# Kernel tuning notes

Hardware: AMD Instinct MI355X
Metric: run time of the kernel (lower is better)

Reference implementation:

```python
import jax, jax.numpy as jnp
import numpy as np
from jax import lax

B = 1024
D_VQ = 64
KS = 1024
KX = 1024
BETA = 0.25


def _conv1d(x, w, b):
    # x: [N, Cin, L], w: [Cout, Cin, 3], 'same' padding
    y = lax.conv_general_dilated(x, w, (1,), [(1, 1)], dimension_numbers=('NCH', 'OIH', 'NCH'))
    return y + b[None, :, None]


def _conv2d(x, w, b):
    # x: [N, Cin, H, W], w: [Cout, Cin, 3, 3], 'same' padding
    y = lax.conv_general_dilated(x, w, (1, 1), [(1, 1), (1, 1)], dimension_numbers=('NCHW', 'OIHW', 'NCHW'))
    return y + b[None, :, None, None]


def _gelu(x):
    return jax.nn.gelu(x, approximate=False)


def _vq_ema(z_e, codebook, beta):
    # z_e: [N, D], codebook: [K, D]
    d = (jnp.sum(z_e * z_e, axis=1, keepdims=True)
         - 2.0 * (z_e @ codebook.T)
         + jnp.sum(codebook * codebook, axis=1)[None, :])  # [N, K]
    idx = jnp.argmin(d, axis=1)                              # [N]
    z_q = codebook[idx]                                      # gather [N, D]
    vq_loss = beta * jnp.mean((z_e - lax.stop_gradient(z_q)) ** 2)
    z_q_st = z_e + lax.stop_gradient(z_q - z_e)              # straight-through
    n = z_e.shape[0]
    probs = jnp.zeros((codebook.shape[0],), z_e.dtype).at[idx].add(1.0) / n
    perplexity = jnp.exp(-jnp.sum(probs * jnp.log(probs + 1e-10)))
    return z_q_st, idx, vq_loss, perplexity


def setup_inputs() -> dict:
    key = jax.random.key(0)
    ks = iter(jax.random.split(key, 40))

    def p(shape, s=0.05):
        return jax.random.normal(next(ks), shape, jnp.float32) * s

    inp = {
        'cubes': jax.random.normal(next(ks), (B, 9, 8, 72), jnp.float32),
        # spectral encoder
        's_w1': p((16, 1, 3)), 's_b1': jnp.zeros((16,), jnp.float32),
        's_w2': p((16, 16, 3)), 's_b2': jnp.zeros((16,), jnp.float32),
        's_fc_w': p((D_VQ, 16 * 8)), 's_fc_b': jnp.zeros((D_VQ,), jnp.float32),
        'cb_s': p((KS, D_VQ), 1.0),
        # spectral decoder
        's_dec_fc_w': p((16 * 8, D_VQ)), 's_dec_fc_b': jnp.zeros((16 * 8,), jnp.float32),
        's_dec_w1': p((16, 16, 3)), 's_dec_b1': jnp.zeros((16,), jnp.float32),
        's_dec_w2': p((1, 16, 3)), 's_dec_b2': jnp.zeros((1,), jnp.float32),
        # spatial encoder
        'x_w1': p((16, 8, 3, 3)), 'x_b1': jnp.zeros((16,), jnp.float32),
        'x_w2': p((16, 16, 3, 3)), 'x_b2': jnp.zeros((16,), jnp.float32),
        'x_fc_w': p((D_VQ, 16 * 3 * 3)), 'x_fc_b': jnp.zeros((D_VQ,), jnp.float32),
        'cb_x': p((KX, D_VQ), 1.0),
        # spatial decoder
        'x_dec_fc_w': p((16 * 3 * 3, D_VQ)), 'x_dec_fc_b': jnp.zeros((16 * 3 * 3,), jnp.float32),
        'x_dec_w1': p((16, 16, 3, 3)), 'x_dec_b1': jnp.zeros((16,), jnp.float32),
        'x_dec_w2': p((8, 16, 3, 3)), 'x_dec_b2': jnp.zeros((8,), jnp.float32),
        'return_recon': 1,
    }
    return inp


def reference(cubes, s_w1, s_b1, s_w2, s_b2, s_fc_w, s_fc_b, cb_s,
              s_dec_fc_w, s_dec_fc_b, s_dec_w1, s_dec_b1, s_dec_w2, s_dec_b2,
              x_w1, x_b1, x_w2, x_b2, x_fc_w, x_fc_b, cb_x,
              x_dec_fc_w, x_dec_fc_b, x_dec_w1, x_dec_b1, x_dec_w2, x_dec_b2,
              return_recon):
    b, p, t, f = cubes.shape
    n = b * p * t
    c6 = cubes.reshape(b, p, t, 8, 3, 3)                   # [B,P,T,8,3,3]
    cperm = jnp.transpose(c6, (0, 1, 2, 4, 5, 3))          # [B,P,T,3,3,8]

    # --- spectral path ---
    spec = jnp.mean(cperm, axis=(3, 4))                    # [B,P,T,8]
    spec_seq = spec.reshape(n, 1, 8)
    s = _gelu(_conv1d(spec_seq, s_w1, s_b1))
    s = _gelu(_conv1d(s, s_w2, s_b2))
    z_e_s = s.reshape(n, 16 * 8) @ s_fc_w.T + s_fc_b       # [N,D]
    z_q_s, k_idx, vq_loss_s, perplex_s = _vq_ema(z_e_s, cb_s, BETA)
    emb_s = z_q_s.reshape(b, p, t, D_VQ)
    k_idx = k_idx.reshape(b, p, t)

    # --- spatial path ---
    spatial = c6.reshape(n, 8, 3, 3)
    x = _gelu(_conv2d(spatial, x_w1, x_b1))
    x = _gelu(_conv2d(x, x_w2, x_b2))
    z_e_x = x.reshape(n, 16 * 9) @ x_fc_w.T + x_fc_b
    z_q_x, m_idx, vq_loss_x, perplex_x = _vq_ema(z_e_x, cb_x, BETA)
    emb_x = z_q_x.reshape(b, p, t, D_VQ)
    m_idx = m_idx.reshape(b, p, t)

    total = vq_loss_s + vq_loss_x

    if return_recon:
        s_dec = (z_q_s @ s_dec_fc_w.T + s_dec_fc_b).reshape(n, 16, 8)
        s_dec = _gelu(_conv1d(s_dec, s_dec_w1, s_dec_b1))
        recon_s = _conv1d(s_dec, s_dec_w2, s_dec_b2)[:, 0, :].reshape(b, p, t, 8)
        recon_loss_s = jnp.mean((recon_s - spec) ** 2)

        x_dec = (z_q_x @ x_dec_fc_w.T + x_dec_fc_b).reshape(n, 16, 3, 3)
        x_dec = _gelu(_conv2d(x_dec, x_dec_w1, x_dec_b1))
        recon_x = _conv2d(x_dec, x_dec_w2, x_dec_b2)        # [N,8,3,3]
        recon_loss_x = jnp.mean((recon_x - spatial) ** 2)
        recon_loss_total = recon_loss_s + recon_loss_x
    else:
        recon_loss_total = jnp.float32(0.0)

    return (emb_s, emb_x, k_idx, m_idx, total, perplex_s, perplex_x, recon_loss_total)
```

## Files before the change

### kernel.cpp

```cpp
#include <hip/hip_runtime.h>
#include <math.h>

#define NTOK 73728

__device__ __forceinline__ float gelu_f(float x) {
    return 0.5f * x * (1.0f + erff(x * 0.70710678118654752440f));
}

__global__ void k_norms(const float* __restrict__ cb_s, const float* __restrict__ cb_x,
                        double* __restrict__ cn_s, double* __restrict__ cn_x) {
    int i = blockIdx.x * blockDim.x + threadIdx.x;
    if (i >= 2048) return;
    const float* cb = (i < 1024) ? cb_s : cb_x;
    double* cn = (i < 1024) ? cn_s : cn_x;
    int c = i & 1023;
    double s = 0.0;
    for (int k = 0; k < 64; ++k) { double v = (double)cb[c * 64 + k]; s += v * v; }
    cn[c] = s;
}

__global__ void k_transpose(const float* __restrict__ src, float* __restrict__ dst, int E) {
    int i = blockIdx.x * 256 + threadIdx.x;
    if (i >= 64 * E) return;
    int e = i >> 6, d = i & 63;
    dst[i] = src[d * E + e];
}

__global__ void k_weff_s(const float* __restrict__ w1, const float* __restrict__ b1,
                         const float* __restrict__ dfcw, const float* __restrict__ dfcb,
                         float* __restrict__ weffT, float* __restrict__ beff) {
    int idx = blockIdx.x * 256 + threadIdx.x;
    if (idx >= 128 * 64) return;
    int o = idx >> 6, d = idx & 63;
    int c = o >> 3, l = o & 7;
    double acc = 0.0;
    for (int ci = 0; ci < 16; ++ci)
        for (int dd = 0; dd < 3; ++dd) {
            int ll = l + dd - 1;
            if (ll < 0 || ll > 7) continue;
            acc += (double)w1[(c * 16 + ci) * 3 + dd] * (double)dfcw[(ci * 8 + ll) * 64 + d];
        }
    weffT[d * 132 + o] = (float)acc;
    if (o < 4) weffT[d * 132 + 128 + o] = 0.f;
    if (d == 0) {
        double bb = (double)b1[c];
        for (int ci = 0; ci < 16; ++ci)
            for (int dd = 0; dd < 3; ++dd) {
                int ll = l + dd - 1;
                if (ll < 0 || ll > 7) continue;
                bb += (double)w1[(c * 16 + ci) * 3 + dd] * (double)dfcb[ci * 8 + ll];
            }
        beff[o] = (float)bb;
    }
}

__global__ void k_weff_x(const float* __restrict__ w1, const float* __restrict__ b1,
                         const float* __restrict__ dfcw, const float* __restrict__ dfcb,
                         float* __restrict__ weffT, float* __restrict__ beff) {
    int idx = blockIdx.x * 256 + threadIdx.x;
    if (idx >= 144 * 64) return;
    int o = idx >> 6, d = idx & 63;
    int c = o / 9, p = o - c * 9;
    int i = p / 3, j = p % 3;
    double acc = 0.0;
    for (int ci = 0; ci < 16; ++ci)
        for (int di = 0; di < 3; ++di) {
            int ii = i + di - 1; if (ii < 0 || ii > 2) continue;
            for (int dj = 0; dj < 3; ++dj) {
                int jj = j + dj - 1; if (jj < 0 || jj > 2) continue;
                acc += (double)w1[((c * 16 + ci) * 3 + di) * 3 + dj]
                     * (double)dfcw[(ci * 9 + ii * 3 + jj) * 64 + d];
            }
        }
    weffT[d * 148 + o] = (float)acc;
    if (o < 4) weffT[d * 148 + 144 + o] = 0.f;
    if (d == 0) {
        double bb = (double)b1[c];
        for (int ci = 0; ci < 16; ++ci)
            for (int di = 0; di < 3; ++di) {
                int ii = i + di - 1; if (ii < 0 || ii > 2) continue;
                for (int dj = 0; dj < 3; ++dj) {
                    int jj = j + dj - 1; if (jj < 0 || jj > 2) continue;
                    bb += (double)w1[((c * 16 + ci) * 3 + di) * 3 + dj]
                        * (double)dfcb[ci * 9 + ii * 3 + jj];
                }
            }
        beff[o] = (float)bb;
    }
}

__global__ void __launch_bounds__(256) k_spec_enc(
    const float* __restrict__ cubes,
    const float* __restrict__ w1, const float* __restrict__ b1,
    const float* __restrict__ w2, const float* __restrict__ b2,
    const float* __restrict__ fcwT, const float* __restrict__ fcb,
    float* __restrict__ z_out)
{
    __shared__ float S[16 * 8];
    __shared__ float A[16 * 136];
    __shared__ float Bb[16 * 136];
    int tid = threadIdx.x;
    int t = tid >> 4, c = tid & 15;
    if (tid < 128) {
        int tk = tid >> 3, f = tid & 7;
        const float* cu = cubes + ((size_t)blockIdx.x * 16 + tk) * 72 + f * 9;
        float s = 0.f;
        #pragma unroll
        for (int k = 0; k < 9; ++k) s += cu[k];
        S[tk * 8 + f] = s * (1.0f / 9.0f);
    }
    __syncthreads();
    {
        float s0[8];
        *(float4*)&s0[0] = *(const float4*)&S[t * 8];
        *(float4*)&s0[4] = *(const float4*)&S[t * 8 + 4];
        float wa = w1[c * 3 + 0], wb = w1[c * 3 + 1], wc = w1[c * 3 + 2], bb = b1[c];
        #pragma unroll
        for (int l = 0; l < 8; ++l) {
            float v = fmaf(wb, s0[l], bb);
            if (l > 0) v = fmaf(wa, s0[l - 1], v);
            if (l < 7) v = fmaf(wc, s0[l + 1], v);
            A[t * 136 + c * 8 + l] = gelu_f(v);
        }
    }
    __syncthreads();
    {
        float acc[8];
        #pragma unroll
        for (int l = 0; l < 8; ++l) acc[l] = b2[c];
        for (int ci = 0; ci < 16; ++ci) {
            float r[8];
            *(float4*)&r[0] = *(const float4*)&A[t * 136 + ci * 8];
            *(float4*)&r[4] = *(const float4*)&A[t * 136 + ci * 8 + 4];
            float wa = w2[(c * 16 + ci) * 3 + 0], wb = w2[(c * 16 + ci) * 3 + 1], wc = w2[(c * 16 + ci) * 3 + 2];
            #pragma unroll
            for (int l = 0; l < 8; ++l) {
                if (l > 0) acc[l] = fmaf(wa, r[l - 1], acc[l]);
                acc[l] = fmaf(wb, r[l], acc[l]);
                if (l < 7) acc[l] = fmaf(wc, r[l + 1], acc[l]);
            }
        }
        #pragma unroll
        for (int l = 0; l < 8; ++l) Bb[t * 136 + c * 8 + l] = gelu_f(acc[l]);
    }
    __syncthreads();
    {
        float4 zv = make_float4(fcb[c * 4 + 0], fcb[c * 4 + 1], fcb[c * 4 + 2], fcb[c * 4 + 3]);
        #pragma unroll 4
        for (int e = 0; e < 128; ++e) {
            float be = Bb[t * 136 + e];
            float4 wv = *(const float4*)(fcwT + (e << 6) + (c << 2));
            zv.x = fmaf(wv.x, be, zv.x);
            zv.y = fmaf(wv.y, be, zv.y);
            zv.z = fmaf(wv.z, be, zv.z);
            zv.w = fmaf(wv.w, be, zv.w);
        }
        *(float4*)(z_out + ((size_t)blockIdx.x * 16 + t) * 64 + c * 4) = zv;
    }
}

__global__ void __launch_bounds__(256) k_spat_enc(
    const float* __restrict__ cubes,
    const float* __restrict__ w1, const float* __restrict__ b1,
    const float* __restrict__ w2, const float* __restrict__ b2,
    const float* __restrict__ fcwT, const float* __restrict__ fcb,
    float* __restrict__ z_out)
{
    __shared__ float A[16 * 200];
    __shared__ float Bb[16 * 200];
    int tid = threadIdx.x;
    int t = tid >> 4, c = tid & 15;
    for (int u = tid; u < 1152; u += 256) {
        int tk = u / 72, e = u - tk * 72;
        int ci = e / 9, p = e - ci * 9;
        A[tk * 200 + ci * 12 + p] = cubes[(size_t)blockIdx.x * 1152 + u];
    }
    __syncthreads();
    {
        float acc[9];
        #pragma unroll
        for (int p = 0; p < 9; ++p) acc[p] = b1[c];
        for (int ci = 0; ci < 8; ++ci) {
            float r[12];
            *(float4*)&r[0] = *(const float4*)&A[t * 200 + ci * 12];
            *(float4*)&r[4] = *(const float4*)&A[t * 200 + ci * 12 + 4];
            *(float4*)&r[8] = *(const float4*)&A[t * 200 + ci * 12 + 8];
            const float* w = w1 + (c * 8 + ci) * 9;
            #pragma unroll
            for (int p = 0; p < 9; ++p) {
                int i = p / 3, j = p % 3;
                #pragma unroll
                for (int di = 0; di < 3; ++di) {
                    int ii = i + di - 1; if (ii < 0 || ii > 2) continue;
                    #pragma unroll
                    for (int dj = 0; dj < 3; ++dj) {
                        int jj = j + dj - 1; if (jj < 0 || jj > 2) continue;
                        acc[p] = fmaf(w[di * 3 + dj], r[ii * 3 + jj], acc[p]);
                    }
                }
            }
        }
        #pragma unroll
        for (int p = 0; p < 9; ++p) Bb[t * 200 + c * 12 + p] = gelu_f(acc[p]);
    }
// ... 9 lines not shown
            *(float4*)&r[8] = *(const float4*)&Bb[t * 200 + ci * 12 + 8];
            const float* w = w2 + (c * 16 + ci) * 9;
            #pragma unroll
            for (int p = 0; p < 9; ++p) {
                int i = p / 3, j = p % 3;
                #pragma unroll
                for (int di = 0; di < 3; ++di) {
                    int ii = i + di - 1; if (ii < 0 || ii > 2) continue;
                    #pragma unroll
                    for (int dj = 0; dj < 3; ++dj) {
                        int jj = j + dj - 1; if (jj < 0 || jj > 2) continue;
                        acc[p] = fmaf(w[di * 3 + dj], r[ii * 3 + jj], acc[p]);
                    }
                }
            }
        }
        __syncthreads();
        #pragma unroll
        for (int p = 0; p < 9; ++p) A[t * 200 + c * 12 + p] = gelu_f(acc[p]);
    }
    __syncthreads();
    {
        float4 zv = make_float4(fcb[c * 4 + 0], fcb[c * 4 + 1], fcb[c * 4 + 2], fcb[c * 4 + 3]);
        #pragma unroll 4
        for (int e = 0; e < 144; ++e) {
            int ci = e / 9, p = e - ci * 9;
            float be = A[t * 200 + ci * 12 + p];
            float4 wv = *(const float4*)(fcwT + (e << 6) + (c << 2));
            zv.x = fmaf(wv.x, be, zv.x);
            zv.y = fmaf(wv.y, be, zv.y);
            zv.z = fmaf(wv.z, be, zv.z);
            zv.w = fmaf(wv.w, be, zv.w);
        }
        *(float4*)(z_out + ((size_t)blockIdx.x * 16 + t) * 64 + c * 4) = zv;
    }
}

__global__ void __launch_bounds__(256) k_vq(
    float* __restrict__ emb, const float* __restrict__ cb,
    const double* __restrict__ cn,
    float* __restrict__ idx_out, int* __restrict__ hist,
    double* __restrict__ partial)
{
    __shared__ double pbest[4][64];
    __shared__ int pidx[4][64];
    __shared__ int lh[1024];
    int tid = threadIdx.x;
    int w = tid >> 6, l = tid & 63;
    for (int u = tid; u < 1024; u += 256) lh[u] = 0;
    size_t n = (size_t)blockIdx.x * 64 + l;
    float z[64];
    {
        const float4* zp = (const float4*)(emb + n * 64);
        #pragma unroll
        for (int k = 0; k < 16; ++k) *(float4*)&z[k * 4] = zp[k];
    }
    int base = __builtin_amdgcn_readfirstlane(w << 8);
    const float* crb = cb + ((size_t)base << 6);
    const double* cnb = cn + base;
    double best = 1e300; int bi = base;
    for (int cc = 0; cc < 256; ++cc) {
        const float* cr = crb + (cc << 6);
        float d0 = 0.f, d1 = 0.f, d2 = 0.f, d3 = 0.f;
        #pragma unroll
        for (int k = 0; k < 64; k += 4) {
            d0 = fmaf(z[k + 0], cr[k + 0], d0);
            d1 = fmaf(z[k + 1], cr[k + 1], d1);
            d2 = fmaf(z[k + 2], cr[k + 2], d2);
            d3 = fmaf(z[k + 3], cr[k + 3], d3);
        }
        float dot = (d0 + d1) + (d2 + d3);
        double dd = cnb[cc] - 2.0 * (double)dot;
        if (dd < best) { best = dd; bi = base + cc; }
    }
    pbest[w][l] = best; pidx[w][l] = bi;
    __syncthreads();
    if (w == 0) {
        double b = pbest[0][l]; int bj = pidx[0][l];
        #pragma unroll
        for (int q = 1; q < 4; ++q) {
            double d = pbest[q][l];
            if (d < b) { b = d; bj = pidx[q][l]; }
        }
        idx_out[n] = (float)bj;
        float qv[64];
        {
            const float4* cq = (const float4*)(cb + ((size_t)bj << 6));
            #pragma unroll
            for (int k = 0; k < 16; ++k) *(float4*)&qv[k * 4] = cq[k];
        }
        float vs = 0.f;
        #pragma unroll
        for (int k = 0; k < 64; ++k) { float df = z[k] - qv[k]; vs = fmaf(df, df, vs); }
        float4* zo = (float4*)(emb + n * 64);
        #pragma unroll
        for (int k = 0; k < 16; ++k) zo[k] = *(float4*)&qv[k * 4];
        atomicAdd(&lh[bj], 1);
        double s = (double)vs;
        #pragma unroll
        for (int o = 32; o > 0; o >>= 1) s += __shfl_down(s, o);
        if (l == 0) partial[blockIdx.x] = s;
    }
    __syncthreads();
    for (int u = tid; u < 1024; u += 256) if (lh[u] > 0) atomicAdd(&hist[u], lh[u]);
}

__global__ void __launch_bounds__(256) k_spec_dec(
    const float* __restrict__ emb, const float* __restrict__ cubes,
    const float* __restrict__ weffT, const float* __restrict__ beff,
    const float* __restrict__ w2, const float* __restrict__ b2,
    double* __restrict__ partial)
{
    __shared__ float Z[16 * 72];
    __shared__ float Bb[16 * 136];
    __shared__ float S[16 * 8];
    __shared__ double wred[4];
    int tid = threadIdx.x;
    int t = tid >> 4, c = tid & 15;
    {
        int tk = tid >> 4, dq = tid & 15;
        *(float4*)&Z[tk * 72 + dq * 4] =
            *(const float4*)(emb + (size_t)blockIdx.x * 1024 + (size_t)tid * 4);
    }
    if (tid < 128) {
        int tk = tid >> 3, f = tid & 7;
        const float* cu = cubes + ((size_t)blockIdx.x * 16 + tk) * 72 + f * 9;
        float s = 0.f;
        #pragma unroll
        for (int k = 0; k < 9; ++k) s += cu[k];
        S[tk * 8 + f] = s * (1.0f / 9.0f);
    }
    __syncthreads();
    float zr[64];
    #pragma unroll
    for (int k = 0; k < 16; ++k) *(float4*)&zr[k * 4] = *(const float4*)&Z[t * 72 + k * 4];
    {
        float4 a0 = make_float4(0.f, 0.f, 0.f, 0.f);
        float4 a1 = make_float4(0.f, 0.f, 0.f, 0.f);
        #pragma unroll 8
        for (int k = 0; k < 64; ++k) {
            float zk = zr[k];
            float4 w0 = *(const float4*)(weffT + k * 132 + (c << 2));
            float4 w1v = *(const float4*)(weffT + k * 132 + 64 + (c << 2));
            a0.x = fmaf(w0.x, zk, a0.x); a0.y = fmaf(w0.y, zk, a0.y);
            a0.z = fmaf(w0.z, zk, a0.z); a0.w = fmaf(w0.w, zk, a0.w);
            a1.x = fmaf(w1v.x, zk, a1.x); a1.y = fmaf(w1v.y, zk, a1.y);
            a1.z = fmaf(w1v.z, zk, a1.z); a1.w = fmaf(w1v.w, zk, a1.w);
        }
        int o0 = c << 2, o1 = 64 + (c << 2);
        float4 g0 = make_float4(gelu_f(a0.x + beff[o0 + 0]), gelu_f(a0.y + beff[o0 + 1]),
                                gelu_f(a0.z + beff[o0 + 2]), gelu_f(a0.w + beff[o0 + 3]));
        float4 g1 = make_float4(gelu_f(a1.x + beff[o1 + 0]), gelu_f(a1.y + beff[o1 + 1]),
                                gelu_f(a1.z + beff[o1 + 2]), gelu_f(a1.w + beff[o1 + 3]));
        *(float4*)&Bb[t * 136 + o0] = g0;
        *(float4*)&Bb[t * 136 + o1] = g1;
    }
    __syncthreads();
    float acc2 = 0.f;
    {
        int h = c >> 3, pos = c & 7;
        float a = (h == 0) ? b2[0] : 0.f;
        for (int ci = h * 8; ci < h * 8 + 8; ++ci) {
            const float* w = w2 + ci * 3;
            const float* hb = &Bb[t * 136 + ci * 8];
            if (pos > 0) a = fmaf(w[0], hb[pos - 1], a);
            a = fmaf(w[1], hb[pos], a);
            if (pos < 7) a = fmaf(w[2], hb[pos + 1], a);
        }
        a += __shfl_xor(a, 8);
        if (h == 0) { float df = a - S[t * 8 + pos]; acc2 = df * df; }
    }
    double s = (double)acc2;
    #pragma unroll
    for (int o = 32; o > 0; o >>= 1) s += __shfl_down(s, o);
    if ((tid & 63) == 0) wred[tid >> 6] = s;
    __syncthreads();
    if (tid == 0) partial[blockIdx.x] = wred[0] + wred[1] + wred[2] + wred[3];
}

__global__ void __launch_bounds__(256) k_spat_dec(
    const float* __restrict__ emb, const float* __restrict__ cubes,
    const float* __restrict__ weffT, const float* __restrict__ beff,
    const float* __restrict__ w2, const float* __restrict__ b2,
    double* __restrict__ partial)
{
    __shared__ float Z[16 * 72];
    __shared__ float H[16 * 200];
    __shared__ float T[16 * 104];
    __shared__ double wred[4];
    int tid = threadIdx.x;
    int t = tid >> 4, c = tid & 15;
    {
        int tk = tid >> 4, dq = tid & 15;
        *(float4*)&Z[tk * 72 + dq * 4] =
            *(const float4*)(emb + (size_t)blockIdx.x * 1024 + (size_t)tid * 4);
    }
    for (int u = tid; u < 1152; u += 256) {
        int tk = u / 72, e = u - tk * 72;
        int ci = e / 9, p = e - ci * 9;
        T[tk * 104 + ci * 12 + p] = cubes[(size_t)blockIdx.x * 1152 + u];
    }
    __syncthreads();
    float zr[64];
    #pragma unroll
    for (int k = 0; k < 16; ++k) *(float4*)&zr[k * 4] = *(const float4*)&Z[t * 72 + k * 4];
    {
        float4 a0 = make_float4(0.f, 0.f, 0.f, 0.f);
        float4 a1 = make_float4(0.f, 0.f, 0.f, 0.f);
        float4 a2 = make_float4(0.f, 0.f, 0.f, 0.f);
        #pragma unroll 8
        for (int k = 0; k < 64; ++k) {
            float zk = zr[k];
            float4 w0 = *(const float4*)(weffT + k * 148 + (c << 2));
            float4 w1v = *(const float4*)(weffT + k * 148 + 64 + (c << 2));
            float4 w2v = *(const float4*)(weffT + k * 148 + 128 + (c << 2));
            a0.x = fmaf(w0.x, zk, a0.x); a0.y = fmaf(w0.y, zk, a0.y);
            a0.z = fmaf(w0.z, zk, a0.z); a0.w = fmaf(w0.w, zk, a0.w);
            a1.x = fmaf(w1v.x, zk, a1.x); a1.y = fmaf(w1v.y, zk, a1.y);
            a1.z = fmaf(w1v.z, zk, a1.z); a1.w = fmaf(w1v.w, zk, a1.w);
            a2.x = fmaf(w2v.x, zk, a2.x); a2.y = fmaf(w2v.y, zk, a2.y);
            a2.z = fmaf(w2v.z, zk, a2.z); a2.w = fmaf(w2v.w, zk, a2.w);
        }
        float av[12] = {a0.x, a0.y, a0.z, a0.w, a1.x, a1.y, a1.z, a1.w, a2.x, a2.y, a2.z, a2.w};
        #pragma unroll
        for (int q = 0; q < 12; ++q) {
            int o = (c << 2) + ((q >> 2) << 6) + (q & 3);
            int ch = o / 9, p = o - ch * 9;
            H[t * 200 + ch * 12 + p] = gelu_f(av[q] + beff[o]);
        }
    }
    __syncthreads();
    float acc2 = 0.f;
    {
        int co = c >> 1, h = c & 1;
        float accp[9];
        #pragma unroll
        for (int p = 0; p < 9; ++p) accp[p] = (h == 0) ? b2[co] : 0.f;
        for (int ci = h * 8; ci < h * 8 + 8; ++ci) {
            float r[12];
            *(float4*)&r[0] = *(const float4*)&H[t * 200 + ci * 12];
            *(float4*)&r[4] = *(const float4*)&H[t * 200 + ci * 12 + 4];
            *(float4*)&r[8] = *(const float4*)&H[t * 200 + ci * 12 + 8];
            const float* w = w2 + (co * 16 + ci) * 9;
            #pragma unroll
            for (int p = 0; p < 9; ++p) {
                int i = p / 3, j = p % 3;
                #pragma unroll
                for (int di = 0; di < 3; ++di) {
                    int ii = i + di - 1; if (ii < 0 || ii > 2) continue;
                    #pragma unroll
                    for (int dj = 0; dj < 3; ++dj) {
                        int jj = j + dj - 1; if (jj < 0 || jj > 2) continue;
                        accp[p] = fmaf(w[di * 3 + dj], r[ii * 3 + jj], accp[p]);
                    }
                }
            }
        }
        #pragma unroll
        for (int p = 0; p < 9; ++p) {
            float tot = accp[p] + __shfl_xor(accp[p], 1);
            if (h == 0) { float df = tot - T[t * 104 + co * 12 + p]; acc2 = fmaf(df, df, acc2); }
        }
    }
    double s = (double)acc2;
    #pragma unroll
    for (int o = 32; o > 0; o >>= 1) s += __shfl_down(s, o);
    if ((tid & 63) == 0) wred[tid >> 6] = s;
    __syncthreads();
    if (tid == 0) partial[blockIdx.x] = wred[0] + wred[1] + wred[2] + wred[3];
}

__global__ void __launch_bounds__(256) k_final(
    const double* __restrict__ p_vq_s, const double* __restrict__ p_vq_x,
    const double* __restrict__ p_rec_s, const double* __restrict__ p_rec_x,
    const int* __restrict__ hist_s, const int* __restrict__ hist_x,
    const int* __restrict__ rr,
    float* __restrict__ outscal)
{
    __shared__ double wred[4];
    int tid = threadIdx.x;
    auto bred = [&](double v) -> double {
        #pragma unroll
        for (int o = 32; o > 0; o >>= 1) v += __shfl_down(v, o);
        __syncthreads();
        if ((tid & 63) == 0) wred[tid >> 6] = v;
        __syncthreads();
        return wred[0] + wred[1] + wred[2] + wred[3];
    };
    double a;
    a = 0; for (int t = tid; t < 1152; t += 256) a += p_vq_s[t];
    double vq_s = bred(a);
    a = 0; for (int t = tid; t < 1152; t += 256) a += p_vq_x[t];
    double vq_x = bred(a);
    a = 0; for (int t = tid; t < 4608; t += 256) a += p_rec_s[t];
    double rec_s = bred(a);
    a = 0; for (int t = tid; t < 4608; t += 256) a += p_rec_x[t];
    double rec_x = bred(a);
    a = 0;
    for (int t = tid; t < 1024; t += 256) {
        double cnt = (double)hist_s[t];
        if (cnt > 0.0) { double p = cnt / (double)NTOK; a += p * log(p + 1e-10); }
    }
    double ent_s = bred(a);
    a = 0;
    for (int t = tid; t < 1024; t += 256) {
        double cnt = (double)hist_x[t];
        if (cnt > 0.0) { double p = cnt / (double)NTOK; a += p * log(p + 1e-10); }
    }
    double ent_x = bred(a);
    if (tid == 0) {
        double total = 0.25 * (vq_s / 4718592.0 + vq_x / 4718592.0);
        double rec = (rr[0] != 0) ? (rec_s / 589824.0 + rec_x / 5308416.0) : 0.0;
        outscal[0] = (float)total;
        outscal[1] = (float)exp(-ent_s);
        outscal[2] = (float)exp(-ent_x);
        outscal[3] = (float)rec;
    }
}

extern "C" void kernel_launch(void* const* d_in, const int* in_sizes, int n_in,
                              void* d_out, int out_size, void* d_ws, size_t ws_size,
                              hipStream_t stream)
{
    const float* cubes  = (const float*)d_in[0];
    const float* s_w1   = (const float*)d_in[1];
// ... 7 lines not shown
    const float* s_dfcb = (const float*)d_in[9];
    const float* s_dw1  = (const float*)d_in[10];
    const float* s_db1  = (const float*)d_in[11];
    const float* s_dw2  = (const float*)d_in[12];
    const float* s_db2  = (const float*)d_in[13];
    const float* x_w1   = (const float*)d_in[14];
    const float* x_b1   = (const float*)d_in[15];
    const float* x_w2   = (const float*)d_in[16];
    const float* x_b2   = (const float*)d_in[17];
    const float* x_fcw  = (const float*)d_in[18];
    const float* x_fcb  = (const float*)d_in[19];
    const float* cb_x   = (const float*)d_in[20];
    const float* x_dfcw = (const float*)d_in[21];
    const float* x_dfcb = (const float*)d_in[22];
    const float* x_dw1  = (const float*)d_in[23];
    const float* x_db1  = (const float*)d_in[24];
    const float* x_dw2  = (const float*)d_in[25];
    const float* x_db2  = (const float*)d_in[26];
    const int*   rr     = (const int*)d_in[27];

    float* out   = (float*)d_out;
    float* emb_s = out;
    float* emb_x = out + 4718592;
    float* kidx  = out + 9437184;
    float* midx  = out + 9510912;
    float* scal  = out + 9584640;

    char* ws = (char*)d_ws;
    int*    hist_s  = (int*)(ws + 0);
    int*    hist_x  = (int*)(ws + 4096);
    double* cn_s    = (double*)(ws + 8192);
    double* cn_x    = (double*)(ws + 16384);
    double* p_vq_s  = (double*)(ws + 24576);
    double* p_vq_x  = (double*)(ws + 33792);
    double* p_rec_s = (double*)(ws + 43008);
    double* p_rec_x = (double*)(ws + 79872);
    float*  beff_s  = (float*)(ws + 116736);
    float*  beff_x  = (float*)(ws + 117248);
    float*  weffT_s = (float*)(ws + 117888);
    float*  weffT_x = (float*)(ws + 151680);
    float*  fcwT_s  = (float*)(ws + 189568);
    float*  fcwT_x  = (float*)(ws + 222336);

    hipMemsetAsync(d_ws, 0, 8192, stream);
    k_norms<<<16, 128, 0, stream>>>(cb_s, cb_x, cn_s, cn_x);
    k_weff_s<<<32, 256, 0, stream>>>(s_dw1, s_db1, s_dfcw, s_dfcb, weffT_s, beff_s);
    k_weff_x<<<36, 256, 0, stream>>>(x_dw1, x_db1, x_dfcw, x_dfcb, weffT_x, beff_x);
    k_transpose<<<32, 256, 0, stream>>>(s_fcw, fcwT_s, 128);
    k_transpose<<<36, 256, 0, stream>>>(x_fcw, fcwT_x, 144);
    k_spec_enc<<<4608, 256, 0, stream>>>(cubes, s_w1, s_b1, s_w2, s_b2, fcwT_s, s_fcb, emb_s);
    k_spat_enc<<<4608, 256, 0, stream>>>(cubes, x_w1, x_b1, x_w2, x_b2, fcwT_x, x_fcb, emb_x);
    k_vq<<<1152, 256, 0, stream>>>(emb_s, cb_s, cn_s, kidx, hist_s, p_vq_s);
    k_vq<<<1152, 256, 0, stream>>>(emb_x, cb_x, cn_x, midx, hist_x, p_vq_x);
    k_spec_dec<<<4608, 256, 0, stream>>>(emb_s, cubes, weffT_s, beff_s, s_dw2, s_db2, p_rec_s);
    k_spat_dec<<<4608, 256, 0, stream>>>(emb_x, cubes, weffT_x, beff_x, x_dw2, x_db2, p_rec_x);
    k_final<<<1, 256, 0, stream>>>(p_vq_s, p_vq_x, p_rec_s, p_rec_x, hist_s, hist_x, rr, scal);
}
```

Measured before the change: 1.078 ms.

## Fuse encoder, VQ search and decoder into one kernel per path

Merges the five small prep kernels into a single k_prep launch. Fuses each path's encoder, nearest-codebook search and decoder/reconstruction loss into one kernel, so z_e and z_q stay in shared memory instead of round-tripping through global memory. The VQ search now stages 64-codeword tiles transposed in LDS and splits codewords across 16 lanes per token, then reduces with shuffles. The cost is a full codebook sweep per 16-token block (4608 blocks versus 1152 before), more shared memory and register pressure, and more partial sums for k_final to reduce.

```diff
diff --git a/kernel.cpp b/kernel.cpp
--- a/kernel.cpp
+++ b/kernel.cpp
@@ -7,100 +7,110 @@
     return 0.5f * x * (1.0f + erff(x * 0.70710678118654752440f));
 }
 
-__global__ void k_norms(const float* __restrict__ cb_s, const float* __restrict__ cb_x,
-                        double* __restrict__ cn_s, double* __restrict__ cn_x) {
-    int i = blockIdx.x * blockDim.x + threadIdx.x;
-    if (i >= 2048) return;
-    const float* cb = (i < 1024) ? cb_s : cb_x;
-    double* cn = (i < 1024) ? cn_s : cn_x;
-    int c = i & 1023;
-    double s = 0.0;
-    for (int k = 0; k < 64; ++k) { double v = (double)cb[c * 64 + k]; s += v * v; }
-    cn[c] = s;
-}
-
-__global__ void k_transpose(const float* __restrict__ src, float* __restrict__ dst, int E) {
-    int i = blockIdx.x * 256 + threadIdx.x;
-    if (i >= 64 * E) return;
-    int e = i >> 6, d = i & 63;
-    dst[i] = src[d * E + e];
-}
-
-__global__ void k_weff_s(const float* __restrict__ w1, const float* __restrict__ b1,
-                         const float* __restrict__ dfcw, const float* __restrict__ dfcb,
-                         float* __restrict__ weffT, float* __restrict__ beff) {
-    int idx = blockIdx.x * 256 + threadIdx.x;
-    if (idx >= 128 * 64) return;
-    int o = idx >> 6, d = idx & 63;
-    int c = o >> 3, l = o & 7;
-    double acc = 0.0;
-    for (int ci = 0; ci < 16; ++ci)
-        for (int dd = 0; dd < 3; ++dd) {
-            int ll = l + dd - 1;
-            if (ll < 0 || ll > 7) continue;
-            acc += (double)w1[(c * 16 + ci) * 3 + dd] * (double)dfcw[(ci * 8 + ll) * 64 + d];
-        }
-    weffT[d * 132 + o] = (float)acc;
-    if (o < 4) weffT[d * 132 + 128 + o] = 0.f;
-    if (d == 0) {
-        double bb = (double)b1[c];
+__global__ void __launch_bounds__(256) k_prep(
+    const float* __restrict__ cb_s, const float* __restrict__ cb_x,
+    double* __restrict__ cn_s, double* __restrict__ cn_x,
+    const float* __restrict__ s_dw1, const float* __restrict__ s_db1,
+    const float* __restrict__ s_dfcw, const float* __restrict__ s_dfcb,
+    float* __restrict__ weffT_s, float* __restrict__ beff_s,
+    const float* __restrict__ x_dw1, const float* __restrict__ x_db1,
+    const float* __restrict__ x_dfcw, const float* __restrict__ x_dfcb,
+    float* __restrict__ weffT_x, float* __restrict__ beff_x,
+    const float* __restrict__ s_fcw, float* __restrict__ fcwT_s,
+    const float* __restrict__ x_fcw, float* __restrict__ fcwT_x)
+{
+    int bid = blockIdx.x, tid = threadIdx.x;
+    if (bid < 8) {
+        int i = bid * 256 + tid;
+        const float* cb = (i < 1024) ? cb_s : cb_x;
+        double* cn = (i < 1024) ? cn_s : cn_x;
+        int c = i & 1023;
+        double s = 0.0;
+        for (int k = 0; k < 64; ++k) { double v = (double)cb[c * 64 + k]; s += v * v; }
+        cn[c] = s;
+    } else if (bid < 40) {
+        int idx = (bid - 8) * 256 + tid;
+        int o = idx >> 6, d = idx & 63;
+        int c = o >> 3, l = o & 7;
+        double acc = 0.0;
         for (int ci = 0; ci < 16; ++ci)
             for (int dd = 0; dd < 3; ++dd) {
                 int ll = l + dd - 1;
                 if (ll < 0 || ll > 7) continue;
-                bb += (double)w1[(c * 16 + ci) * 3 + dd] * (double)dfcb[ci * 8 + ll];
-            }
-        beff[o] = (float)bb;
-    }
-}
-
-__global__ void k_weff_x(const float* __restrict__ w1, const float* __restrict__ b1,
-                         const float* __restrict__ dfcw, const float* __restrict__ dfcb,
-                         float* __restrict__ weffT, float* __restrict__ beff) {
-    int idx = blockIdx.x * 256 + threadIdx.x;
-    if (idx >= 144 * 64) return;
-    int o = idx >> 6, d = idx & 63;
-    int c = o / 9, p = o - c * 9;
-    int i = p / 3, j = p % 3;
-    double acc = 0.0;
-    for (int ci = 0; ci < 16; ++ci)
-        for (int di = 0; di < 3; ++di) {
-            int ii = i + di - 1; if (ii < 0 || ii > 2) continue;
-            for (int dj = 0; dj < 3; ++dj) {
-                int jj = j + dj - 1; if (jj < 0 || jj > 2) continue;
-                acc += (double)w1[((c * 16 + ci) * 3 + di) * 3 + dj]
-                     * (double)dfcw[(ci * 9 + ii * 3 + jj) * 64 + d];
-            }
-        }
-    weffT[d * 148 + o] = (float)acc;
-    if (o < 4) weffT[d * 148 + 144 + o] = 0.f;
-    if (d == 0) {
-        double bb = (double)b1[c];
+                acc += (double)s_dw1[(c * 16 + ci) * 3 + dd] * (double)s_dfcw[(ci * 8 + ll) * 64 + d];
+            }
+        weffT_s[d * 132 + o] = (float)acc;
+        if (o < 4) weffT_s[d * 132 + 128 + o] = 0.f;
+        if (d == 0) {
+            double bb = (double)s_db1[c];
+            for (int ci = 0; ci < 16; ++ci)
+                for (int dd = 0; dd < 3; ++dd) {
+                    int ll = l + dd - 1;
+                    if (ll < 0 || ll > 7) continue;
+                    bb += (double)s_dw1[(c * 16 + ci) * 3 + dd] * (double)s_dfcb[ci * 8 + ll];
+                }
+            beff_s[o] = (float)bb;
+        }
+    } else if (bid < 76) {
+        int idx = (bid - 40) * 256 + tid;
+        int o = idx >> 6, d = idx & 63;
+        int c = o / 9, p = o - c * 9;
+        int i = p / 3, j = p % 3;
+        double acc = 0.0;
         for (int ci = 0; ci < 16; ++ci)
             for (int di = 0; di < 3; ++di) {
                 int ii = i + di - 1; if (ii < 0 || ii > 2) continue;
                 for (int dj = 0; dj < 3; ++dj) {
                     int jj = j + dj - 1; if (jj < 0 || jj > 2) continue;
-                    bb += (double)w1[((c * 16 + ci) * 3 + di) * 3 + dj]
-                        * (double)dfcb[ci * 9 + ii * 3 + jj];
+                    acc += (double)x_dw1[((c * 16 + ci) * 3 + di) * 3 + dj]
+                         * (double)x_dfcw[(ci * 9 + ii * 3 + jj) * 64 + d];
                 }
             }
-        beff[o] = (float)bb;
+        weffT_x[d * 148 + o] = (float)acc;
+        if (o < 4) weffT_x[d * 148 + 144 + o] = 0.f;
+        if (d == 0) {
+            double bb = (double)x_db1[c];
+            for (int ci = 0; ci < 16; ++ci)
+                for (int di = 0; di < 3; ++di) {
+                    int ii = i + di - 1; if (ii < 0 || ii > 2) continue;
+                    for (int dj = 0; dj < 3; ++dj) {
+                        int jj = j + dj - 1; if (jj < 0 || jj > 2) continue;
+                        bb += (double)x_dw1[((c * 16 + ci) * 3 + di) * 3 + dj]
+                            * (double)x_dfcb[ci * 9 + ii * 3 + jj];
+                    }
+                }
+            beff_x[o] = (float)bb;
+        }
+    } else if (bid < 108) {
+        int i = (bid - 76) * 256 + tid;
+        fcwT_s[i] = s_fcw[(i & 63) * 128 + (i >> 6)];
+    } else {
+        int i = (bid - 108) * 256 + tid;
+        fcwT_x[i] = x_fcw[(i & 63) * 144 + (i >> 6)];
     }
 }
 
-__global__ void __launch_bounds__(256) k_spec_enc(
+__global__ void __launch_bounds__(256) k_spec_fused(
     const float* __restrict__ cubes,
     const float* __restrict__ w1, const float* __restrict__ b1,
     const float* __restrict__ w2, const float* __restrict__ b2,
     const float* __restrict__ fcwT, const float* __restrict__ fcb,
-    float* __restrict__ z_out)
+    const float* __restrict__ cb, const double* __restrict__ cn,
+    const float* __restrict__ weffT, const float* __restrict__ beff,
+    const float* __restrict__ dw2, const float* __restrict__ db2,
+    float* __restrict__ emb, float* __restrict__ idx_out,
+    int* __restrict__ hist, double* __restrict__ p_vq, double* __restrict__ p_rec)
 {
+    __shared__ float SM[4352];
+    __shared__ float Z[16 * 68];
     __shared__ float S[16 * 8];
-    __shared__ float A[16 * 136];
-    __shared__ float Bb[16 * 136];
+    __shared__ double CNt[64];
+    __shared__ double wred[4];
     int tid = threadIdx.x;
     int t = tid >> 4, c = tid & 15;
+    float* A = SM;
+    float* Bb = SM + 2176;
+
     if (tid < 128) {
         int tk = tid >> 3, f = tid & 7;
         const float* cu = cubes + ((size_t)blockIdx.x * 16 + tk) * 72 + f * 9;
@@ -155,21 +165,159 @@
             zv.z = fmaf(wv.z, be, zv.z);
             zv.w = fmaf(wv.w, be, zv.w);
         }
-        *(float4*)(z_out + ((size_t)blockIdx.x * 16 + t) * 64 + c * 4) = zv;
+        *(float4*)&Z[t * 68 + (c << 2)] = zv;
+    }
+    __syncthreads();
+
+    float z[64];
+    #pragma unroll
+    for (int k = 0; k < 16; ++k) *(float4*)&z[k * 4] = *(const float4*)&Z[t * 68 + k * 4];
+    double best = 1e300; int bi = 0;
+    for (int tile = 0; tile < 16; ++tile) {
+        __syncthreads();
+        {
+            const float* src = cb + ((size_t)tile << 12);
+            #pragma unroll
+            for (int j = 0; j < 4; ++j) {
+                int f = tid + (j << 8);
+                int r = f >> 4;
+                int k4 = (f & 15) << 2;
+                float4 v = *(const float4*)(src + (r << 6) + k4);
+                SM[(k4 + 0) * 68 + r] = v.x;
+                SM[(k4 + 1) * 68 + r] = v.y;
+                SM[(k4 + 2) * 68 + r] = v.z;
+                SM[(k4 + 3) * 68 + r] = v.w;
+            }
+            if (tid < 64) CNt[tid] = cn[(tile << 6) + tid];
+        }
+        __syncthreads();
+        float d0[4], d1[4], d2[4], d3[4];
+        #pragma unroll
+        for (int q = 0; q < 4; ++q) { d0[q] = 0.f; d1[q] = 0.f; d2[q] = 0.f; d3[q] = 0.f; }
+        #pragma unroll
+        for (int k = 0; k < 64; ++k) {
+            float4 v = *(const float4*)&SM[k * 68 + (c << 2)];
+            float zk = z[k];
+            d0[k & 3] = fmaf(zk, v.x, d0[k & 3]);
+            d1[k & 3] = fmaf(zk, v.y, d1[k & 3]);
+            d2[k & 3] = fmaf(zk, v.z, d2[k & 3]);
+            d3[k & 3] = fmaf(zk, v.w, d3[k & 3]);
+        }
+        int cb0 = (tile << 6) + (c << 2);
+        {
+            float dot = (d0[0] + d0[1]) + (d0[2] + d0[3]);
+            double dd = CNt[(c << 2) + 0] - 2.0 * (double)dot;
+            if (dd < best) { best = dd; bi = cb0 + 0; }
+        }
+        {
+            float dot = (d1[0] + d1[1]) + (d1[2] + d1[3]);
+            double dd = CNt[(c << 2) + 1] - 2.0 * (double)dot;
+            if (dd < best) { best = dd; bi = cb0 + 1; }
+        }
+        {
+            float dot = (d2[0] + d2[1]) + (d2[2] + d2[3]);
+            double dd = CNt[(c << 2) + 2] - 2.0 * (double)dot;
+            if (dd < best) { best = dd; bi = cb0 + 2; }
+        }
+        {
+            float dot = (d3[0] + d3[1]) + (d3[2] + d3[3]);
+            double dd = CNt[(c << 2) + 3] - 2.0 * (double)dot;
+            if (dd < best) { best = dd; bi = cb0 + 3; }
+        }
+    }
+    #pragma unroll
+    for (int m = 1; m < 16; m <<= 1) {
+        double ob = __shfl_xor(best, m);
+        int oi = __shfl_xor(bi, m);
+        if (ob < best || (ob == best && oi < bi)) { best = ob; bi = oi; }
+    }
+
+    size_t n = (size_t)blockIdx.x * 16 + t;
+    float4 q4 = *(const float4*)(cb + ((size_t)bi << 6) + (c << 2));
+    float4 zq = *(const float4*)&Z[t * 68 + (c << 2)];
+    float dx = zq.x - q4.x, dy = zq.y - q4.y, dz = zq.z - q4.z, dw = zq.w - q4.w;
+    float vp = fmaf(dw, dw, fmaf(dz, dz, fmaf(dy, dy, dx * dx)));
+    *(float4*)(emb + n * 64 + (c << 2)) = q4;
+    if (c == 0) { idx_out[n] = (float)bi; atomicAdd(&hist[bi], 1); }
+    *(float4*)&Z[t * 68 + (c << 2)] = q4;
+    {
+        double s = (double)vp;
+        #pragma unroll
+        for (int o = 32; o > 0; o >>= 1) s += __shfl_down(s, o);
+        if ((tid & 63) == 0) wred[tid >> 6] = s;
+        __syncthreads();
+        if (tid == 0) p_vq[blockIdx.x] = wred[0] + wred[1] + wred[2] + wred[3];
+    }
+
+    float zr[64];
+    #pragma unroll
+    for (int k = 0; k < 16; ++k) *(float4*)&zr[k * 4] = *(const float4*)&Z[t * 68 + k * 4];
+    {
+        float4 a0 = make_float4(0.f, 0.f, 0.f, 0.f);
+        float4 a1 = make_float4(0.f, 0.f, 0.f, 0.f);
+        #pragma unroll
+        for (int k = 0; k < 64; ++k) {
+            float zk = zr[k];
+            float4 w0 = *(const float4*)(weffT + k * 132 + (c << 2));
+            float4 w1v = *(const float4*)(weffT + k * 132 + 64 + (c << 2));
+            a0.x = fmaf(w0.x, zk, a0.x); a0.y = fmaf(w0.y, zk, a0.y);
+            a0.z = fmaf(w0.z, zk, a0.z); a0.w = fmaf(w0.w, zk, a0.w);
+            a1.x = fmaf(w1v.x, zk, a1.x); a1.y = fmaf(w1v.y, zk, a1.y);
+            a1.z = fmaf(w1v.z, zk, a1.z); a1.w = fmaf(w1v.w, zk, a1.w);
+        }
+        int o0 = c << 2, o1 = 64 + (c << 2);
+        float4 g0 = make_float4(gelu_f(a0.x + beff[o0 + 0]), gelu_f(a0.y + beff[o0 + 1]),
+                                gelu_f(a0.z + beff[o0 + 2]), gelu_f(a0.w + beff[o0 + 3]));
+        float4 g1 = make_float4(gelu_f(a1.x + beff[o1 + 0]), gelu_f(a1.y + beff[o1 + 1]),
+                                gelu_f(a1.z + beff[o1 + 2]), gelu_f(a1.w + beff[o1 + 3]));
+        *(float4*)&SM[t * 136 + o0] = g0;
+        *(float4*)&SM[t * 136 + o1] = g1;
+    }
+    __syncthreads();
+    float acc2 = 0.f;
+    {
+        int h = c >> 3, pos = c & 7;
+        float a = (h == 0) ? db2[0] : 0.f;
+        for (int ci = h * 8; ci < h * 8 + 8; ++ci) {
+            const float* w = dw2 + ci * 3;
+            const float* hb = &SM[t * 136 + ci * 8];
+            if (pos > 0) a = fmaf(w[0], hb[pos - 1], a);
+            a = fmaf(w[1], hb[pos], a);
+            if (pos < 7) a = fmaf(w[2], hb[pos + 1], a);
+        }
+        a += __shfl_xor(a, 8);
+        if (h == 0) { float df = a - S[t * 8 + pos]; acc2 = df * df; }
+    }
+    {
+        double s = (double)acc2;
+        #pragma unroll
+        for (int o = 32; o > 0; o >>= 1) s += __shfl_down(s, o);
+        if ((tid & 63) == 0) wred[tid >> 6] = s;
+        __syncthreads();
+        if (tid == 0) p_rec[blockIdx.x] = wred[0] + wred[1] + wred[2] + wred[3];
     }
 }
 
-__global__ void __launch_bounds__(256) k_spat_enc(
+__global__ void __launch_bounds__(256) k_spat_fused(
     const float* __restrict__ cubes,
     const float* __restrict__ w1, const float* __restrict__ b1,
     const float* __restrict__ w2, const float* __restrict__ b2,
     const float* __restrict__ fcwT, const float* __restrict__ fcb,
-    float* __restrict__ z_out)
+    const float* __restrict__ cb, const double* __restrict__ cn,
+    const float* __restrict__ weffT, const float* __restrict__ beff,
+    const float* __restrict__ dw2, const float* __restrict__ db2,
+    float* __restrict__ emb, float* __restrict__ idx_out,
+    int* __restrict__ hist, double* __restrict__ p_vq, double* __restrict__ p_rec)
 {
-    __shared__ float A[16 * 200];
-    __shared__ float Bb[16 * 200];
+    __shared__ float SM[6400];
+    __shared__ float Z[16 * 68];
+    __shared__ double CNt[64];
+    __shared__ double wred[4];
     int tid = threadIdx.x;
     int t = tid >> 4, c = tid & 15;
+    float* A = SM;
+    float* Bb = SM + 3200;
+
     for (int u = tid; u < 1152; u += 256) {
         int tk = u / 72, e = u - tk * 72;
         int ci = e / 9, p = e - ci * 9;
@@ -245,183 +393,98 @@
             zv.z = fmaf(wv.z, be, zv.z);
             zv.w = fmaf(wv.w, be, zv.w);
         }
-        *(float4*)(z_out + ((size_t)blockIdx.x * 16 + t) * 64 + c * 4) = zv;
-    }
-}
-
-__global__ void __launch_bounds__(256) k_vq(
-    float* __restrict__ emb, const float* __restrict__ cb,
-    const double* __restrict__ cn,
-    float* __restrict__ idx_out, int* __restrict__ hist,
-    double* __restrict__ partial)
-{
-    __shared__ double pbest[4][64];
-    __shared__ int pidx[4][64];
-    __shared__ int lh[1024];
-    int tid = threadIdx.x;
-    int w = tid >> 6, l = tid & 63;
-    for (int u = tid; u < 1024; u += 256) lh[u] = 0;
-    size_t n = (size_t)blockIdx.x * 64 + l;
+        *(float4*)&Z[t * 68 + (c << 2)] = zv;
+    }
+    __syncthreads();
+
     float z[64];
-    {
-        const float4* zp = (const float4*)(emb + n * 64);
-        #pragma unroll
-        for (int k = 0; k < 16; ++k) *(float4*)&z[k * 4] = zp[k];
-    }
-    int base = __builtin_amdgcn_readfirstlane(w << 8);
-    const float* crb = cb + ((size_t)base << 6);
-    const double* cnb = cn + base;
-    double best = 1e300; int bi = base;
-    for (int cc = 0; cc < 256; ++cc) {
-        const float* cr = crb + (cc << 6);
-        float d0 = 0.f, d1 = 0.f, d2 = 0.f, d3 = 0.f;
-        #pragma unroll
-        for (int k = 0; k < 64; k += 4) {
-            d0 = fmaf(z[k + 0], cr[k + 0], d0);
-            d1 = fmaf(z[k + 1], cr[k + 1], d1);
-            d2 = fmaf(z[k + 2], cr[k + 2], d2);
-            d3 = fmaf(z[k + 3], cr[k + 3], d3);
-        }
-        float dot = (d0 + d1) + (d2 + d3);
-        double dd = cnb[cc] - 2.0 * (double)dot;
-        if (dd < best) { best = dd; bi = base + cc; }
-    }
-    pbest[w][l] = best; pidx[w][l] = bi;
-    __syncthreads();
-    if (w == 0) {
-        double b = pbest[0][l]; int bj = pidx[0][l];
-        #pragma unroll
-        for (int q = 1; q < 4; ++q) {
-            double d = pbest[q][l];
-            if (d < b) { b = d; bj = pidx[q][l]; }
-        }
-        idx_out[n] = (float)bj;
-        float qv[64];
-        {
-            const float4* cq = (const float4*)(cb + ((size_t)bj << 6));
+    #pragma unroll
+    for (int k = 0; k < 16; ++k) *(float4*)&z[k * 4] = *(const float4*)&Z[t * 68 + k * 4];
+    double best = 1e300; int bi = 0;
+    for (int tile = 0; tile < 16; ++tile) {
+        __syncthreads();
+        {
+            const float* src = cb + ((size_t)tile << 12);
             #pragma unroll
-            for (int k = 0; k < 16; ++k) *(float4*)&qv[k * 4] = cq[k];
-        }
-        float vs = 0.f;
-        #pragma unroll
-        for (int k = 0; k < 64; ++k) { float df = z[k] - qv[k]; vs = fmaf(df, df, vs); }
-        float4* zo = (float4*)(emb + n * 64);
-        #pragma unroll
-        for (int k = 0; k < 16; ++k) zo[k] = *(float4*)&qv[k * 4];
-        atomicAdd(&lh[bj], 1);
-        double s = (double)vs;
+            for (int j = 0; j < 4; ++j) {
+                int f = tid + (j << 8);
+                int r = f >> 4;
+                int k4 = (f & 15) << 2;
+                float4 v = *(const float4*)(src + (r << 6) + k4);
+                SM[(k4 + 0) * 68 + r] = v.x;
+                SM[(k4 + 1) * 68 + r] = v.y;
+                SM[(k4 + 2) * 68 + r] = v.z;
+                SM[(k4 + 3) * 68 + r] = v.w;
+            }
+            if (tid < 64) CNt[tid] = cn[(tile << 6) + tid];
+        }
+        __syncthreads();
+        float d0[4], d1[4], d2[4], d3[4];
+        #pragma unroll
+        for (int q = 0; q < 4; ++q) { d0[q] = 0.f; d1[q] = 0.f; d2[q] = 0.f; d3[q] = 0.f; }
+        #pragma unroll
+        for (int k = 0; k < 64; ++k) {
+            float4 v = *(const float4*)&SM[k * 68 + (c << 2)];
+            float zk = z[k];
+            d0[k & 3] = fmaf(zk, v.x, d0[k & 3]);
+            d1[k & 3] = fmaf(zk, v.y, d1[k & 3]);
+            d2[k & 3] = fmaf(zk, v.z, d2[k & 3]);
+            d3[k & 3] = fmaf(zk, v.w, d3[k & 3]);
+        }
+        int cb0 = (tile << 6) + (c << 2);
+        {
+            float dot = (d0[0] + d0[1]) + (d0[2] + d0[3]);
+            double dd = CNt[(c << 2) + 0] - 2.0 * (double)dot;
+            if (dd < best) { best = dd; bi = cb0 + 0; }
+        }
+        {
+            float dot = (d1[0] + d1[1]) + (d1[2] + d1[3]);
+            double dd = CNt[(c << 2) + 1] - 2.0 * (double)dot;
+            if (dd < best) { best = dd; bi = cb0 + 1; }
+        }
+        {
+            float dot = (d2[0] + d2[1]) + (d2[2] + d2[3]);
+            double dd = CNt[(c << 2) + 2] - 2.0 * (double)dot;
+            if (dd < best) { best = dd; bi = cb0 + 2; }
+        }
+        {
+            float dot = (d3[0] + d3[1]) + (d3[2] + d3[3]);
+            double dd = CNt[(c << 2) + 3] - 2.0 * (double)dot;
+            if (dd < best) { best = dd; bi = cb0 + 3; }
+        }
+    }
+    #pragma unroll
+    for (int m = 1; m < 16; m <<= 1) {
+        double ob = __shfl_xor(best, m);
+        int oi = __shfl_xor(bi, m);
+        if (ob < best || (ob == best && oi < bi)) { best = ob; bi = oi; }
+    }
+
+    size_t n = (size_t)blockIdx.x * 16 + t;
+    float4 q4 = *(const float4*)(cb + ((size_t)bi << 6) + (c << 2));
+    float4 zq = *(const float4*)&Z[t * 68 + (c << 2)];
+    float dx = zq.x - q4.x, dy = zq.y - q4.y, dz = zq.z - q4.z, dw = zq.w - q4.w;
+    float vp = fmaf(dw, dw, fmaf(dz, dz, fmaf(dy, dy, dx * dx)));
+    *(float4*)(emb + n * 64 + (c << 2)) = q4;
+    if (c == 0) { idx_out[n] = (float)bi; atomicAdd(&hist[bi], 1); }
+    *(float4*)&Z[t * 68 + (c << 2)] = q4;
+    {
+        double s = (double)vp;
         #pragma unroll
         for (int o = 32; o > 0; o >>= 1) s += __shfl_down(s, o);
-        if (l == 0) partial[blockIdx.x] = s;
-    }
-    __syncthreads();
-    for (int u = tid; u < 1024; u += 256) if (lh[u] > 0) atomicAdd(&hist[u], lh[u]);
-}
-
-__global__ void __launch_bounds__(256) k_spec_dec(
-    const float* __restrict__ emb, const float* __restrict__ cubes,
-    const float* __restrict__ weffT, const float* __restrict__ beff,
-    const float* __restrict__ w2, const float* __restrict__ b2,
-    double* __restrict__ partial)
-{
-    __shared__ float Z[16 * 72];
-    __shared__ float Bb[16 * 136];
-    __shared__ float S[16 * 8];
-    __shared__ double wred[4];
-    int tid = threadIdx.x;
-    int t = tid >> 4, c = tid & 15;
-    {
-        int tk = tid >> 4, dq = tid & 15;
-        *(float4*)&Z[tk * 72 + dq * 4] =
-            *(const float4*)(emb + (size_t)blockIdx.x * 1024 + (size_t)tid * 4);
-    }
-    if (tid < 128) {
-        int tk = tid >> 3, f = tid & 7;
-        const float* cu = cubes + ((size_t)blockIdx.x * 16 + tk) * 72 + f * 9;
-        float s = 0.f;
-        #pragma unroll
-        for (int k = 0; k < 9; ++k) s += cu[k];
-        S[tk * 8 + f] = s * (1.0f / 9.0f);
-    }
-    __syncthreads();
+        if ((tid & 63) == 0) wred[tid >> 6] = s;
+        __syncthreads();
+        if (tid == 0) p_vq[blockIdx.x] = wred[0] + wred[1] + wred[2] + wred[3];
+    }
+
     float zr[64];
     #pragma unroll
-    for (int k = 0; k < 16; ++k) *(float4*)&zr[k * 4] = *(const float4*)&Z[t * 72 + k * 4];
-    {
-        float4 a0 = make_float4(0.f, 0.f, 0.f, 0.f);
-        float4 a1 = make_float4(0.f, 0.f, 0.f, 0.f);
-        #pragma unroll 8
-        for (int k = 0; k < 64; ++k) {
-            float zk = zr[k];
-            float4 w0 = *(const float4*)(weffT + k * 132 + (c << 2));
-            float4 w1v = *(const float4*)(weffT + k * 132 + 64 + (c << 2));
-            a0.x = fmaf(w0.x, zk, a0.x); a0.y = fmaf(w0.y, zk, a0.y);
-            a0.z = fmaf(w0.z, zk, a0.z); a0.w = fmaf(w0.w, zk, a0.w);
-            a1.x = fmaf(w1v.x, zk, a1.x); a1.y = fmaf(w1v.y, zk, a1.y);
-            a1.z = fmaf(w1v.z, zk, a1.z); a1.w = fmaf(w1v.w, zk, a1.w);
-        }
-        int o0 = c << 2, o1 = 64 + (c << 2);
-        float4 g0 = make_float4(gelu_f(a0.x + beff[o0 + 0]), gelu_f(a0.y + beff[o0 + 1]),
-                                gelu_f(a0.z + beff[o0 + 2]), gelu_f(a0.w + beff[o0 + 3]));
-        float4 g1 = make_float4(gelu_f(a1.x + beff[o1 + 0]), gelu_f(a1.y + beff[o1 + 1]),
-                                gelu_f(a1.z + beff[o1 + 2]), gelu_f(a1.w + beff[o1 + 3]));
-        *(float4*)&Bb[t * 136 + o0] = g0;
-        *(float4*)&Bb[t * 136 + o1] = g1;
-    }
-    __syncthreads();
-    float acc2 = 0.f;
-    {
-        int h = c >> 3, pos = c & 7;
-        float a = (h == 0) ? b2[0] : 0.f;
-        for (int ci = h * 8; ci < h * 8 + 8; ++ci) {
-            const float* w = w2 + ci * 3;
-            const float* hb = &Bb[t * 136 + ci * 8];
-            if (pos > 0) a = fmaf(w[0], hb[pos - 1], a);
-            a = fmaf(w[1], hb[pos], a);
-            if (pos < 7) a = fmaf(w[2], hb[pos + 1], a);
-        }
-        a += __shfl_xor(a, 8);
-        if (h == 0) { float df = a - S[t * 8 + pos]; acc2 = df * df; }
-    }
-    double s = (double)acc2;
-    #pragma unroll
-    for (int o = 32; o > 0; o >>= 1) s += __shfl_down(s, o);
-    if ((tid & 63) == 0) wred[tid >> 6] = s;
-    __syncthreads();
-    if (tid == 0) partial[blockIdx.x] = wred[0] + wred[1] + wred[2] + wred[3];
-}
-
-__global__ void __launch_bounds__(256) k_spat_dec(
-    const float* __restrict__ emb, const float* __restrict__ cubes,
-    const float* __restrict__ weffT, const float* __restrict__ beff,
-    const float* __restrict__ w2, const float* __restrict__ b2,
-    double* __restrict__ partial)
-{
-    __shared__ float Z[16 * 72];
-    __shared__ float H[16 * 200];
-    __shared__ float T[16 * 104];
-    __shared__ double wred[4];
-    int tid = threadIdx.x;
-    int t = tid >> 4, c = tid & 15;
-    {
-        int tk = tid >> 4, dq = tid & 15;
-        *(float4*)&Z[tk * 72 + dq * 4] =
-            *(const float4*)(emb + (size_t)blockIdx.x * 1024 + (size_t)tid * 4);
-    }
-    for (int u = tid; u < 1152; u += 256) {
-        int tk = u / 72, e = u - tk * 72;
-        int ci = e / 9, p = e - ci * 9;
-        T[tk * 104 + ci * 12 + p] = cubes[(size_t)blockIdx.x * 1152 + u];
-    }
-    __syncthreads();
-    float zr[64];
-    #pragma unroll
-    for (int k = 0; k < 16; ++k) *(float4*)&zr[k * 4] = *(const float4*)&Z[t * 72 + k * 4];
+    for (int k = 0; k < 16; ++k) *(float4*)&zr[k * 4] = *(const float4*)&Z[t * 68 + k * 4];
     {
         float4 a0 = make_float4(0.f, 0.f, 0.f, 0.f);
         float4 a1 = make_float4(0.f, 0.f, 0.f, 0.f);
         float4 a2 = make_float4(0.f, 0.f, 0.f, 0.f);
-        #pragma unroll 8
+        #pragma unroll
         for (int k = 0; k < 64; ++k) {
             float zk = zr[k];
             float4 w0 = *(const float4*)(weffT + k * 148 + (c << 2));
@@ -439,7 +502,7 @@
         for (int q = 0; q < 12; ++q) {
             int o = (c << 2) + ((q >> 2) << 6) + (q & 3);
             int ch = o / 9, p = o - ch * 9;
-            H[t * 200 + ch * 12 + p] = gelu_f(av[q] + beff[o]);
+            SM[t * 200 + ch * 12 + p] = gelu_f(av[q] + beff[o]);
         }
     }
     __syncthreads();
@@ -448,13 +511,13 @@
         int co = c >> 1, h = c & 1;
         float accp[9];
         #pragma unroll
-        for (int p = 0; p < 9; ++p) accp[p] = (h == 0) ? b2[co] : 0.f;
+        for (int p = 0; p < 9; ++p) accp[p] = (h == 0) ? db2[co] : 0.f;
         for (int ci = h * 8; ci < h * 8 + 8; ++ci) {
             float r[12];
-            *(float4*)&r[0] = *(const float4*)&H[t * 200 + ci * 12];
-            *(float4*)&r[4] = *(const float4*)&H[t * 200 + ci * 12 + 4];
-            *(float4*)&r[8] = *(const float4*)&H[t * 200 + ci * 12 + 8];
-            const float* w = w2 + (co * 16 + ci) * 9;
+            *(float4*)&r[0] = *(const float4*)&SM[t * 200 + ci * 12];
+            *(float4*)&r[4] = *(const float4*)&SM[t * 200 + ci * 12 + 4];
+            *(float4*)&r[8] = *(const float4*)&SM[t * 200 + ci * 12 + 8];
+            const float* w = dw2 + (co * 16 + ci) * 9;
             #pragma unroll
             for (int p = 0; p < 9; ++p) {
                 int i = p / 3, j = p % 3;
@@ -469,18 +532,21 @@
                 }
             }
         }
+        const float* cu = cubes + n * 72 + co * 9;
         #pragma unroll
         for (int p = 0; p < 9; ++p) {
             float tot = accp[p] + __shfl_xor(accp[p], 1);
-            if (h == 0) { float df = tot - T[t * 104 + co * 12 + p]; acc2 = fmaf(df, df, acc2); }
-        }
-    }
-    double s = (double)acc2;
-    #pragma unroll
-    for (int o = 32; o > 0; o >>= 1) s += __shfl_down(s, o);
-    if ((tid & 63) == 0) wred[tid >> 6] = s;
-    __syncthreads();
-    if (tid == 0) partial[blockIdx.x] = wred[0] + wred[1] + wred[2] + wred[3];
+            if (h == 0) { float df = tot - cu[p]; acc2 = fmaf(df, df, acc2); }
+        }
+    }
+    {
+        double s = (double)acc2;
+        #pragma unroll
+        for (int o = 32; o > 0; o >>= 1) s += __shfl_down(s, o);
+        if ((tid & 63) == 0) wred[tid >> 6] = s;
+        __syncthreads();
+        if (tid == 0) p_rec[blockIdx.x] = wred[0] + wred[1] + wred[2] + wred[3];
+    }
 }
 
 __global__ void __launch_bounds__(256) k_final(
@@ -501,9 +567,9 @@
         return wred[0] + wred[1] + wred[2] + wred[3];
     };
     double a;
-    a = 0; for (int t = tid; t < 1152; t += 256) a += p_vq_s[t];
+    a = 0; for (int t = tid; t < 4608; t += 256) a += p_vq_s[t];
     double vq_s = bred(a);
-    a = 0; for (int t = tid; t < 1152; t += 256) a += p_vq_x[t];
+    a = 0; for (int t = tid; t < 4608; t += 256) a += p_vq_x[t];
     double vq_x = bred(a);
     a = 0; for (int t = tid; t < 4608; t += 256) a += p_rec_s[t];
     double rec_s = bred(a);
@@ -577,27 +643,26 @@
     double* cn_s    = (double*)(ws + 8192);
     double* cn_x    = (double*)(ws + 16384);
     double* p_vq_s  = (double*)(ws + 24576);
-    double* p_vq_x  = (double*)(ws + 33792);
-    double* p_rec_s = (double*)(ws + 43008);
-    double* p_rec_x = (double*)(ws + 79872);
-    float*  beff_s  = (float*)(ws + 116736);
-    float*  beff_x  = (float*)(ws + 117248);
-    float*  weffT_s = (float*)(ws + 117888);
-    float*  weffT_x = (float*)(ws + 151680);
-    float*  fcwT_s  = (float*)(ws + 189568);
-    float*  fcwT_x  = (float*)(ws + 222336);
+    double* p_vq_x  = (double*)(ws + 61440);
+    double* p_rec_s = (double*)(ws + 98304);
+    double* p_rec_x = (double*)(ws + 135168);
+    float*  beff_s  = (float*)(ws + 172032);
+    float*  beff_x  = (float*)(ws + 172544);
+    float*  weffT_s = (float*)(ws + 173120);
+    float*  weffT_x = (float*)(ws + 206912);
+    float*  fcwT_s  = (float*)(ws + 244800);
+    float*  fcwT_x  = (float*)(ws + 277568);
 
     hipMemsetAsync(d_ws, 0, 8192, stream);
-    k_norms<<<16, 128, 0, stream>>>(cb_s, cb_x, cn_s, cn_x);
-    k_weff_s<<<32, 256, 0, stream>>>(s_dw1, s_db1, s_dfcw, s_dfcb, weffT_s, beff_s);
-    k_weff_x<<<36, 256, 0, stream>>>(x_dw1, x_db1, x_dfcw, x_dfcb, weffT_x, beff_x);
-    k_transpose<<<32, 256, 0, stream>>>(s_fcw, fcwT_s, 128);
-    k_transpose<<<36, 256, 0, stream>>>(x_fcw, fcwT_x, 144);
-    k_spec_enc<<<4608, 256, 0, stream>>>(cubes, s_w1, s_b1, s_w2, s_b2, fcwT_s, s_fcb, emb_s);
-    k_spat_enc<<<4608, 256, 0, stream>>>(cubes, x_w1, x_b1, x_w2, x_b2, fcwT_x, x_fcb, emb_x);
-    k_vq<<<1152, 256, 0, stream>>>(emb_s, cb_s, cn_s, kidx, hist_s, p_vq_s);
-    k_vq<<<1152, 256, 0, stream>>>(emb_x, cb_x, cn_x, midx, hist_x, p_vq_x);
-    k_spec_dec<<<4608, 256, 0, stream>>>(emb_s, cubes, weffT_s, beff_s, s_dw2, s_db2, p_rec_s);
-    k_spat_dec<<<4608, 256, 0, stream>>>(emb_x, cubes, weffT_x, beff_x, x_dw2, x_db2, p_rec_x);
+    k_prep<<<144, 256, 0, stream>>>(cb_s, cb_x, cn_s, cn_x,
+                                    s_dw1, s_db1, s_dfcw, s_dfcb, weffT_s, beff_s,
+                                    x_dw1, x_db1, x_dfcw, x_dfcb, weffT_x, beff_x,
+                                    s_fcw, fcwT_s, x_fcw, fcwT_x);
+    k_spec_fused<<<4608, 256, 0, stream>>>(cubes, s_w1, s_b1, s_w2, s_b2, fcwT_s, s_fcb,
+                                           cb_s, cn_s, weffT_s, beff_s, s_dw2, s_db2,
+                                           emb_s, kidx, hist_s, p_vq_s, p_rec_s);
+    k_spat_fused<<<4608, 256, 0, stream>>>(cubes, x_w1, x_b1, x_w2, x_b2, fcwT_x, x_fcb,
+                                           cb_x, cn_x, weffT_x, beff_x, x_dw2, x_db2,
+                                           emb_x, midx, hist_x, p_vq_x, p_rec_x);
     k_final<<<1, 256, 0, stream>>>(p_vq_s, p_vq_x, p_rec_s, p_rec_x, hist_s, hist_x, rr, scal);
 }
```

Result: slower. 4.125 ms (+282.5%).
